# Kernel optimization log

Hardware: AMD Instinct MI355X
Metric: run time of the kernel (lower is better)

## Reference

```python
import jax, jax.numpy as jnp
import numpy as np

N_NODES = 100000
N_EDGES = 1600000
IN_CH = 64
HIDDEN = 64
OUT_DIM = HIDDEN // 2  # 32


def setup_inputs() -> dict:
    key = jax.random.key(0)
    ks = jax.random.split(key, 10)
    x = jax.random.normal(ks[0], (N_NODES, IN_CH), dtype=jnp.float32)
    edge_index = jax.random.randint(ks[1], (2, N_EDGES), 0, N_NODES, dtype=jnp.int64)
    s = 1.0 / np.sqrt(IN_CH)
    sh = 1.0 / np.sqrt(HIDDEN)
    # SAGEConv layer 1: lin_l (with bias) on aggregated neighbors, lin_r (no bias) on root
    w1l = jax.random.uniform(ks[2], (HIDDEN, IN_CH), jnp.float32, -s, s)
    b1 = jax.random.uniform(ks[3], (HIDDEN,), jnp.float32, -s, s)
    w1r = jax.random.uniform(ks[4], (HIDDEN, IN_CH), jnp.float32, -s, s)
    # SAGEConv layer 2
    w2l = jax.random.uniform(ks[5], (HIDDEN, HIDDEN), jnp.float32, -sh, sh)
    b2 = jax.random.uniform(ks[6], (HIDDEN,), jnp.float32, -sh, sh)
    w2r = jax.random.uniform(ks[7], (HIDDEN, HIDDEN), jnp.float32, -sh, sh)
    # readout head
    wh = jax.random.uniform(ks[8], (OUT_DIM, HIDDEN), jnp.float32, -sh, sh)
    bh = jax.random.uniform(ks[9], (OUT_DIM,), jnp.float32, -sh, sh)
    return {"x": x, "edge_index": edge_index, "w1l": w1l, "b1": b1, "w1r": w1r,
            "w2l": w2l, "b2": b2, "w2r": w2r, "wh": wh, "bh": bh}


def _sage_conv(h, src, dst, wl, bl, wr):
    # mean-aggregate messages from src nodes onto dst nodes
    msg = h[src]                                            # [E, d]
    agg = jax.ops.segment_sum(msg, dst, num_segments=N_NODES)  # [N, d]
    deg = jax.ops.segment_sum(jnp.ones((msg.shape[0],), h.dtype), dst,
                              num_segments=N_NODES)            # [N]
    mean = agg / jnp.maximum(deg, 1.0)[:, None]
    return mean @ wl.T + bl + h @ wr.T


def reference(x, edge_index, w1l, b1, w1r, w2l, b2, w2r, wh, bh):
    src, dst = edge_index[0], edge_index[1]
    # dropout layers are identity in eval mode
    h = jax.nn.relu(_sage_conv(x, src, dst, w1l, b1, w1r))
    h = jax.nn.relu(_sage_conv(h, src, dst, w2l, b2, w2r))
    return h @ wh.T + bh
```

## Files before the change

kernel.cpp:

```cpp
#include <hip/hip_runtime.h>


#define D 64
#define OUTD 32
#define REG_SHIFT 8
#define REG_SIZE 256
#define BCHUNK 4096
#define PADQ 16
#define CAP 5120
#define OUTCAP 8960

#define OFF_FLAG     0
#define OFF_RCUR     64
#define OFF_DEG      576
#define OFF_ROWSTART 100928
#define OFF_INV      201280
#define OFF_COL      301632
#define OFF_EBUF     3804992
#define OFF_H1B      7005056
#define OFF_MEANB    10205120
#define OFF_WC1      13405120
#define OFF_WC2      13409216
#define OFF_WHB      13413312

typedef __attribute__((ext_vector_type(8))) short bf16x8;
typedef __attribute__((ext_vector_type(4))) float f32x4;

__device__ __forceinline__ unsigned short bf16rne(float x) {
    unsigned u = __float_as_uint(x);
    unsigned r = (u + 0x7FFFu + ((u >> 16) & 1u)) >> 16;
    return (unsigned short)r;
}

__global__ void detect_init(const int* __restrict__ e32, int* __restrict__ flag,
                            int* __restrict__ rcur, int NR) {
    int t = threadIdx.x;
    if (t < 64) {
        int v = e32[2 * t + 1];
        unsigned long long m = __ballot(v != 0);
        if (t == 0) flag[0] = (m == 0ULL) ? 1 : 0;
    }
    if (t < NR) rcur[t] = t * CAP;
}

__global__ __launch_bounds__(256) void bin_edges(
        const int* __restrict__ e32, const int* __restrict__ flag,
        int* __restrict__ rcur, int* __restrict__ ebuf, int E, int NR) {
    __shared__ int stage[BCHUNK];
    __shared__ unsigned short rgn[BCHUNK];
    __shared__ int hist[512], lbase[512], startr[512], s1[512];
    int t = threadIdx.x;
    int mode = flag[0];
    int base = blockIdx.x * BCHUNK;
    for (int i = t; i < 512; i += 256) hist[i] = 0;
    __syncthreads();
    for (int j = t; j < BCHUNK; j += 256) {
        int i = base + j;
        if (i < E) {
            int d = mode ? e32[2 * (E + i)] : e32[E + i];
            atomicAdd(&hist[d >> REG_SHIFT], 1);
        }
    }
    __syncthreads();
    {
        int* a = lbase; int* b = s1;
        for (int i = t; i < 512; i += 256) a[i] = hist[i];
        __syncthreads();
        for (int off = 1; off < 512; off <<= 1) {
            for (int i = t; i < 512; i += 256)
                b[i] = a[i] + ((i >= off) ? a[i - off] : 0);
            __syncthreads();
            int* tmp = a; a = b; b = tmp;
        }
        for (int i = t; i < 512; i += 256) {
            int incl = a[i];
            int ex = incl - hist[i];
            __syncthreads();
            lbase[i] = ex;
        }
        __syncthreads();
    }
    for (int i = t; i < 512; i += 256) {
        int st = 0;
        if (i < NR && hist[i] > 0) {
            st = atomicAdd(&rcur[i], hist[i]);
            int lim = (i + 1) * CAP - hist[i];
            if (st > lim) st = lim;
        }
        startr[i] = st;
    }
    __syncthreads();
    for (int i = t; i < 512; i += 256) hist[i] = 0;
    __syncthreads();
    for (int j = t; j < BCHUNK; j += 256) {
        int i = base + j;
        if (i < E) {
            int s = mode ? e32[2 * i]       : e32[i];
            int d = mode ? e32[2 * (E + i)] : e32[E + i];
            int r = d >> REG_SHIFT;
            int o = atomicAdd(&hist[r], 1);
            int pos = lbase[r] + o;
            stage[pos] = ((d & (REG_SIZE - 1)) << 24) | s;
            rgn[pos] = (unsigned short)r;
        }
    }
    __syncthreads();
    int count = E - base; if (count > BCHUNK) count = BCHUNK;
    for (int i = t; i < count; i += 256) {
        int r = rgn[i];
        ebuf[startr[r] + (i - lbase[r])] = stage[i];
    }
}

__global__ __launch_bounds__(256) void build_csr(
        const int* __restrict__ ebuf, const int* __restrict__ rcur,
        int* __restrict__ degP, int* __restrict__ rowStartP, float* __restrict__ inv,
        int* __restrict__ colP, int N) {
    __shared__ int hist[REG_SIZE], cur[REG_SIZE], sA[REG_SIZE], sB[REG_SIZE];
    int r = blockIdx.x;
    int t = threadIdx.x;
    int lo = r << REG_SHIFT;
    int e0 = r * CAP, e1 = rcur[r];
    int colPbase = r * OUTCAP;
    hist[t] = 0;
    __syncthreads();
    for (int i = e0 + t; i < e1; i += 256)
        atomicAdd(&hist[((unsigned)ebuf[i]) >> 24], 1);
    __syncthreads();
    int v = hist[t];
    int vp = (v + PADQ - 1) & ~(PADQ - 1);
    int* a = sA; int* b = sB;
    a[t] = vp;
    __syncthreads();
    for (int off = 1; off < 256; off <<= 1) {
        b[t] = a[t] + ((t >= off) ? a[t - off] : 0);
        __syncthreads();
        int* tmp = a; a = b; b = tmp;
    }
    int startP = colPbase + (a[t] - vp);
    int node = lo + t;
    if (node < N) {
        degP[node] = vp;
        rowStartP[node] = startP;
        inv[node] = 1.0f / (float)(v > 0 ? v : 1);
    }
    cur[t] = startP;
    __syncthreads();
    for (int i = e0 + t; i < e1; i += 256) {
        int p = ebuf[i];
        int pos = atomicAdd(&cur[((unsigned)p) >> 24], 1);
        colP[pos] = (p & 0xFFFFFF) << 7;
    }
    __syncthreads();
    int zoff = N << 7;
    for (int k = startP + v; k < startP + vp; ++k) colP[k] = zoff;
}

__global__ void prep_all(const float* __restrict__ x, unsigned short* __restrict__ xb,
                         unsigned short* __restrict__ h1b,
                         const float* __restrict__ w1l, const float* __restrict__ w1r,
                         const float* __restrict__ w2l, const float* __restrict__ w2r,
                         const float* __restrict__ wh,
                         unsigned short* __restrict__ wcat1,
                         unsigned short* __restrict__ wcat2,
                         unsigned short* __restrict__ whb, int n4, int N) {
    int i = blockIdx.x * 256 + threadIdx.x;
    if (i < n4) {
        float4 v = ((const float4*)x)[i];
        unsigned lo = (unsigned)bf16rne(v.x) | ((unsigned)bf16rne(v.y) << 16);
        unsigned hi = (unsigned)bf16rne(v.z) | ((unsigned)bf16rne(v.w) << 16);
        ((uint2*)xb)[i] = make_uint2(lo, hi);
        return;
    }
    int j = i - n4;
    if (j < 16) {
        ((uint2*)xb)[(size_t)N * 16 + j] = make_uint2(0u, 0u);
    } else if (j < 32) {
        ((uint2*)h1b)[(size_t)N * 16 + (j - 16)] = make_uint2(0u, 0u);
    } else if (j < 32 + 8192) {
        int q = j - 32;
        int o = q >> 7, k = q & 127;
        wcat1[q] = bf16rne(k < 64 ? w1l[o * 64 + k] : w1r[o * 64 + k - 64]);
    } else if (j < 32 + 16384) {
        int q = j - 32 - 8192;
        int o = q >> 7, k = q & 127;
        wcat2[q] = bf16rne(k < 64 ? w2l[o * 64 + k] : w2r[o * 64 + k - 64]);
    } else if (j < 32 + 16384 + 2048) {
        int q = j - 32 - 16384;
        whb[q] = bf16rne(wh[q]);
    }
}

__global__ __launch_bounds__(256, 8) void gather_mean_bf16(
        const unsigned short* __restrict__ hb, const int* __restrict__ rowStartP,
        const int* __restrict__ degPv, const int* __restrict__ colP,
        const float* __restrict__ invdeg, unsigned short* __restrict__ meanb,
        int n) {
    int wid = (blockIdx.x * 256 + (int)threadIdx.x) >> 6;
    int lane = threadIdx.x & 63;
    if (wid >= n) return;
    int node = __builtin_amdgcn_readfirstlane(wid);

    int rs = rowStartP[node];
    int dgp = degPv[node];
    const char* hbC = (const char*)hb;

    float a0 = 0.f, a1 = 0.f, a2 = 0.f, a3 = 0.f;
    float a4 = 0.f, a5 = 0.f, a6 = 0.f, a7 = 0.f;

    for (int base = 0; base < dgp; base += 64) {
        int cv = colP[rs + base + lane];
        int m = dgp - base; if (m > 64) m = 64;
        for (int p = 0; p < m; p += 16) {
#define G(j, A) { \
            int cb = __builtin_amdgcn_readlane(cv, p + (j)); \
            const unsigned short* rp = (const unsigned short*)(hbC + cb); \
            unsigned u = rp[lane]; \
            A += __uint_as_float(u << 16); }
            G(0, a0)  G(1, a1)  G(2, a2)  G(3, a3)
            G(4, a4)  G(5, a5)  G(6, a6)  G(7, a7)
            G(8, a0)  G(9, a1)  G(10, a2) G(11, a3)
            G(12, a4) G(13, a5) G(14, a6) G(15, a7)
#undef G
        }
    }
    float s = ((a0 + a1) + (a2 + a3)) + ((a4 + a5) + (a6 + a7));
    meanb[(size_t)node * 64 + lane] = bf16rne(s * invdeg[node]);
}

template <bool HEAD>
__global__ __launch_bounds__(256, 2) void dense_mfma(
        const unsigned short* __restrict__ meanb,
        const unsigned short* __restrict__ ownb,
        const unsigned short* __restrict__ wcat,
        const float* __restrict__ bias,
        unsigned short* __restrict__ houtb,
        const unsigned short* __restrict__ whb,
        const float* __restrict__ bh,
        float* __restrict__ outp,
        int n) {
    const int lane = threadIdx.x & 63;
    const int wave = threadIdx.x >> 6;
    const int l15 = lane & 15;
    const int kg  = lane >> 4;

    bf16x8 Bf[4][4];
#pragma unroll
    for (int nt = 0; nt < 4; ++nt)
#pragma unroll
        for (int s = 0; s < 4; ++s)
            Bf[nt][s] = *(const bf16x8*)(wcat + (nt * 16 + l15) * 128 + s * 32 + kg * 8);

    float biasc[4];
#pragma unroll
    for (int nt = 0; nt < 4; ++nt) biasc[nt] = bias[nt * 16 + l15];

    bf16x8 Hf[2][2];
    float bhc[2];
    if constexpr (HEAD) {
#pragma unroll
        for (int nt = 0; nt < 2; ++nt) {
#pragma unroll
            for (int s = 0; s < 2; ++s)
                Hf[nt][s] = *(const bf16x8*)(whb + (nt * 16 + l15) * 64 + s * 32 + kg * 8);
            bhc[nt] = bh[nt * 16 + l15];
        }
    }

    __shared__ unsigned short hlds[HEAD ? 4 * 16 * 64 : 64];

    const int ntiles = (n + 15) >> 4;
    const int stride = gridDim.x * 4;
    int tile = blockIdx.x * 4 + wave;
    if (tile >= ntiles) return;

    bf16x8 Ac[4], An[4];
    {
        int row = tile * 16 + l15; if (row >= n) row = n - 1;
        const unsigned short* mrow = meanb + (size_t)row * 64 + kg * 8;
        const unsigned short* orow = ownb  + (size_t)row * 64 + kg * 8;
        Ac[0] = *(const bf16x8*)(mrow);
        Ac[1] = *(const bf16x8*)(mrow + 32);
        Ac[2] = *(const bf16x8*)(orow);
        Ac[3] = *(const bf16x8*)(orow + 32);
    }

    while (true) {
        int nxt = tile + stride;
        bool hasNext = nxt < ntiles;
        if (hasNext) {
            int row = nxt * 16 + l15; if (row >= n) row = n - 1;
            const unsigned short* mrow = meanb + (size_t)row * 64 + kg * 8;
            const unsigned short* orow = ownb  + (size_t)row * 64 + kg * 8;
            An[0] = *(const bf16x8*)(mrow);
            An[1] = *(const bf16x8*)(mrow + 32);
            An[2] = *(const bf16x8*)(orow);
            An[3] = *(const bf16x8*)(orow + 32);
        }

        f32x4 acc[4];
#pragma unroll
        for (int nt = 0; nt < 4; ++nt) {
            f32x4 a = {biasc[nt], biasc[nt], biasc[nt], biasc[nt]};
            a = __builtin_amdgcn_mfma_f32_16x16x32_bf16(Ac[0], Bf[nt][0], a, 0, 0, 0);
            a = __builtin_amdgcn_mfma_f32_16x16x32_bf16(Ac[1], Bf[nt][1], a, 0, 0, 0);
            a = __builtin_amdgcn_mfma_f32_16x16x32_bf16(Ac[2], Bf[nt][2], a, 0, 0, 0);
            a = __builtin_amdgcn_mfma_f32_16x16x32_bf16(Ac[3], Bf[nt][3], a, 0, 0, 0);
            acc[nt] = a;
        }

        int nb = tile * 16;
        if constexpr (!HEAD) {
#pragma unroll
            for (int nt = 0; nt < 4; ++nt)
#pragma unroll
                for (int r = 0; r < 4; ++r) {
                    int row = nb + kg * 4 + r;
                    float h = fmaxf(acc[nt][r], 0.0f);
                    if (row < n) houtb[(size_t)row * 64 + nt * 16 + l15] = bf16rne(h);
                }
        } else {
            unsigned short* L = hlds + wave * 1024;
            int n7 = lane & 7;
#pragma unroll
            for (int nt = 0; nt < 4; ++nt) {
                int bGlob = nt * 2 + (l15 >> 3);
#pragma unroll
                for (int r = 0; r < 4; ++r) {
                    int m = kg * 4 + r;
                    float h = fmaxf(acc[nt][r], 0.0f);
                    L[m * 64 + ((bGlob ^ (m & 7)) * 8) + n7] = bf16rne(h);
                }
            }
            __builtin_amdgcn_wave_barrier();
            bf16x8 hA[2];
#pragma unroll
            for (int s = 0; s < 2; ++s) {
                int kb = s * 4 + kg;
                hA[s] = *(const bf16x8*)(L + l15 * 64 + ((kb ^ (l15 & 7)) * 8));
            }
            __builtin_amdgcn_wave_barrier();
            f32x4 acc2[2];
#pragma unroll
            for (int nt = 0; nt < 2; ++nt) {
                f32x4 a = {bhc[nt], bhc[nt], bhc[nt], bhc[nt]};
                a = __builtin_amdgcn_mfma_f32_16x16x32_bf16(hA[0], Hf[nt][0], a, 0, 0, 0);
                a = __builtin_amdgcn_mfma_f32_16x16x32_bf16(hA[1], Hf[nt][1], a, 0, 0, 0);
                acc2[nt] = a;
            }
#pragma unroll
            for (int nt = 0; nt < 2; ++nt)
#pragma unroll
                for (int r = 0; r < 4; ++r) {
                    int row = nb + kg * 4 + r;
                    if (row < n) outp[(size_t)row * 32 + nt * 16 + l15] = acc2[nt][r];
                }
        }

        if (!hasNext) break;
        tile = nxt;
#pragma unroll
        for (int q = 0; q < 4; ++q) Ac[q] = An[q];
    }
}

extern "C" void kernel_launch(void* const* d_in, const int* in_sizes, int n_in,
                              void* d_out, int out_size, void* d_ws, size_t ws_size,
                              hipStream_t stream) {
    const float* x   = (const float*)d_in[0];
    const int* edges = (const int*)d_in[1];
    const float* w1l = (const float*)d_in[2];
    const float* b1  = (const float*)d_in[3];
    const float* w1r = (const float*)d_in[4];
    const float* w2l = (const float*)d_in[5];
    const float* b2  = (const float*)d_in[6];
    const float* w2r = (const float*)d_in[7];
    const float* wh  = (const float*)d_in[8];
    const float* bh  = (const float*)d_in[9];
    float* out = (float*)d_out;

    const int N = in_sizes[0] / D;
    const int E = in_sizes[1] / 2;
    const int NR = (N + REG_SIZE - 1) >> REG_SHIFT;

    int* ws = (int*)d_ws;
    int*            flag     = ws + OFF_FLAG;
    int*            rcur     = ws + OFF_RCUR;
    int*            degP     = ws + OFF_DEG;
    int*            rowStartP= ws + OFF_ROWSTART;
    float*          inv      = (float*)(ws + OFF_INV);
    int*            colP     = ws + OFF_COL;
    int*            ebuf     = ws + OFF_EBUF;
    unsigned short* xb       = (unsigned short*)(ws + OFF_EBUF);
    unsigned short* h1b      = (unsigned short*)(ws + OFF_H1B);
    unsigned short* meanb    = (unsigned short*)(ws + OFF_MEANB);
    unsigned short* wcat1    = (unsigned short*)(ws + OFF_WC1);
    unsigned short* wcat2    = (unsigned short*)(ws + OFF_WC2);
    unsigned short* whb      = (unsigned short*)(ws + OFF_WHB);

    detect_init<<<1, 512, 0, stream>>>(edges, flag, rcur, NR);
    int bblocks = (E + BCHUNK - 1) / BCHUNK;
    bin_edges<<<bblocks, 256, 0, stream>>>(edges, flag, rcur, ebuf, E, NR);
    build_csr<<<NR, 256, 0, stream>>>(ebuf, rcur, degP, rowStartP, inv, colP, N);

    int n4 = N * D / 4;
    prep_all<<<(n4 + 32 + 16384 + 2048 + 255) / 256, 256, 0, stream>>>(
        x, xb, h1b, w1l, w1r, w2l, w2r, wh, wcat1, wcat2, whb, n4, N);

    int gblocks = (N + 3) / 4;
    int ntiles = (N + 15) / 16;
    int dblocks = (ntiles + 7) / 8;

    gather_mean_bf16<<<gblocks, 256, 0, stream>>>(xb, rowStartP, degP, colP, inv,
                                                  meanb, N);
    dense_mfma<false><<<dblocks, 256, 0, stream>>>(meanb, xb, wcat1, b1,
                                                   h1b, nullptr, nullptr, nullptr, N);
    gather_mean_bf16<<<gblocks, 256, 0, stream>>>(h1b, rowStartP, degP, colP, inv,
                                                  meanb, N);
    dense_mfma<true><<<dblocks, 256, 0, stream>>>(meanb, h1b, wcat2, b2,
                                                  nullptr, whb, bh, out, N);
}
```

Measured before the change: 164.1 us.

## Fuse bf16 prep into edge binning kernel and gather two neighbors per wave

The separate x/weight bf16 conversion kernel is folded into the edge binning launch as extra blocks, which needs xb moved to its own workspace region so it no longer aliases ebuf. This removes one launch and lets conversion overlap with binning. The gather kernel now has each half-wave load a different neighbor row as 4-byte (two-bf16) words, so one instruction covers two edges. Each half keeps its own accumulators, and the halves are combined with a cross-half shuffle before a packed store. The costs are more accumulator registers, shuffles instead of readlanes, and a larger workspace.

```diff
diff --git a/kernel.cpp b/kernel.cpp
--- a/kernel.cpp
+++ b/kernel.cpp
@@ -17,11 +17,12 @@
 #define OFF_INV      201280
 #define OFF_COL      301632
 #define OFF_EBUF     3804992
-#define OFF_H1B      7005056
-#define OFF_MEANB    10205120
-#define OFF_WC1      13405120
-#define OFF_WC2      13409216
-#define OFF_WHB      13413312
+#define OFF_XB       5806912
+#define OFF_H1B      9006944
+#define OFF_MEANB    12206976
+#define OFF_WC1      15406976
+#define OFF_WC2      15411072
+#define OFF_WHB      15415168
 
 typedef __attribute__((ext_vector_type(8))) short bf16x8;
 typedef __attribute__((ext_vector_type(4))) float f32x4;
@@ -43,13 +44,50 @@
     if (t < NR) rcur[t] = t * CAP;
 }
 
-__global__ __launch_bounds__(256) void bin_edges(
+__global__ __launch_bounds__(256) void bin_prep(
         const int* __restrict__ e32, const int* __restrict__ flag,
-        int* __restrict__ rcur, int* __restrict__ ebuf, int E, int NR) {
+        int* __restrict__ rcur, int* __restrict__ ebuf, int E, int NR, int bblocks,
+        const float* __restrict__ x, unsigned short* __restrict__ xb,
+        unsigned short* __restrict__ h1b,
+        const float* __restrict__ w1l, const float* __restrict__ w1r,
+        const float* __restrict__ w2l, const float* __restrict__ w2r,
+        const float* __restrict__ wh,
+        unsigned short* __restrict__ wcat1, unsigned short* __restrict__ wcat2,
+        unsigned short* __restrict__ whb, int n4, int N) {
     __shared__ int stage[BCHUNK];
     __shared__ unsigned short rgn[BCHUNK];
     __shared__ int hist[512], lbase[512], startr[512], s1[512];
     int t = threadIdx.x;
+
+    if (blockIdx.x >= bblocks) {
+        int i = (blockIdx.x - bblocks) * 256 + t;
+        if (i < n4) {
+            float4 v = ((const float4*)x)[i];
+            unsigned lo = (unsigned)bf16rne(v.x) | ((unsigned)bf16rne(v.y) << 16);
+            unsigned hi = (unsigned)bf16rne(v.z) | ((unsigned)bf16rne(v.w) << 16);
+            ((uint2*)xb)[i] = make_uint2(lo, hi);
+            return;
+        }
+        int j = i - n4;
+        if (j < 16) {
+            ((uint2*)xb)[(size_t)N * 16 + j] = make_uint2(0u, 0u);
+        } else if (j < 32) {
+            ((uint2*)h1b)[(size_t)N * 16 + (j - 16)] = make_uint2(0u, 0u);
+        } else if (j < 32 + 8192) {
+            int q = j - 32;
+            int o = q >> 7, k = q & 127;
+            wcat1[q] = bf16rne(k < 64 ? w1l[o * 64 + k] : w1r[o * 64 + k - 64]);
+        } else if (j < 32 + 16384) {
+            int q = j - 32 - 8192;
+            int o = q >> 7, k = q & 127;
+            wcat2[q] = bf16rne(k < 64 ? w2l[o * 64 + k] : w2r[o * 64 + k - 64]);
+        } else if (j < 32 + 16384 + 2048) {
+            int q = j - 32 - 16384;
+            whb[q] = bf16rne(wh[q]);
+        }
+        return;
+    }
+
     int mode = flag[0];
     int base = blockIdx.x * BCHUNK;
     for (int i = t; i < 512; i += 256) hist[i] = 0;
@@ -156,41 +194,6 @@
     for (int k = startP + v; k < startP + vp; ++k) colP[k] = zoff;
 }
 
-__global__ void prep_all(const float* __restrict__ x, unsigned short* __restrict__ xb,
-                         unsigned short* __restrict__ h1b,
-                         const float* __restrict__ w1l, const float* __restrict__ w1r,
-                         const float* __restrict__ w2l, const float* __restrict__ w2r,
-                         const float* __restrict__ wh,
-                         unsigned short* __restrict__ wcat1,
-                         unsigned short* __restrict__ wcat2,
-                         unsigned short* __restrict__ whb, int n4, int N) {
-    int i = blockIdx.x * 256 + threadIdx.x;
-    if (i < n4) {
-        float4 v = ((const float4*)x)[i];
-        unsigned lo = (unsigned)bf16rne(v.x) | ((unsigned)bf16rne(v.y) << 16);
-        unsigned hi = (unsigned)bf16rne(v.z) | ((unsigned)bf16rne(v.w) << 16);
-        ((uint2*)xb)[i] = make_uint2(lo, hi);
-        return;
-    }
-    int j = i - n4;
-    if (j < 16) {
-        ((uint2*)xb)[(size_t)N * 16 + j] = make_uint2(0u, 0u);
-    } else if (j < 32) {
-        ((uint2*)h1b)[(size_t)N * 16 + (j - 16)] = make_uint2(0u, 0u);
-    } else if (j < 32 + 8192) {
-        int q = j - 32;
-        int o = q >> 7, k = q & 127;
-        wcat1[q] = bf16rne(k < 64 ? w1l[o * 64 + k] : w1r[o * 64 + k - 64]);
-    } else if (j < 32 + 16384) {
-        int q = j - 32 - 8192;
-        int o = q >> 7, k = q & 127;
-        wcat2[q] = bf16rne(k < 64 ? w2l[o * 64 + k] : w2r[o * 64 + k - 64]);
-    } else if (j < 32 + 16384 + 2048) {
-        int q = j - 32 - 16384;
-        whb[q] = bf16rne(wh[q]);
-    }
-}
-
 __global__ __launch_bounds__(256, 8) void gather_mean_bf16(
         const unsigned short* __restrict__ hb, const int* __restrict__ rowStartP,
         const int* __restrict__ degPv, const int* __restrict__ colP,
@@ -204,28 +207,38 @@
     int rs = rowStartP[node];
     int dgp = degPv[node];
     const char* hbC = (const char*)hb;
-
-    float a0 = 0.f, a1 = 0.f, a2 = 0.f, a3 = 0.f;
-    float a4 = 0.f, a5 = 0.f, a6 = 0.f, a7 = 0.f;
+    int half = lane >> 5, l31 = lane & 31;
+    int voff = l31 << 2;
+
+    float aL0 = 0.f, aL1 = 0.f, aL2 = 0.f, aL3 = 0.f;
+    float aL4 = 0.f, aL5 = 0.f, aL6 = 0.f, aL7 = 0.f;
+    float aH0 = 0.f, aH1 = 0.f, aH2 = 0.f, aH3 = 0.f;
+    float aH4 = 0.f, aH5 = 0.f, aH6 = 0.f, aH7 = 0.f;
 
     for (int base = 0; base < dgp; base += 64) {
         int cv = colP[rs + base + lane];
         int m = dgp - base; if (m > 64) m = 64;
-        for (int p = 0; p < m; p += 16) {
-#define G(j, A) { \
-            int cb = __builtin_amdgcn_readlane(cv, p + (j)); \
-            const unsigned short* rp = (const unsigned short*)(hbC + cb); \
-            unsigned u = rp[lane]; \
-            A += __uint_as_float(u << 16); }
-            G(0, a0)  G(1, a1)  G(2, a2)  G(3, a3)
-            G(4, a4)  G(5, a5)  G(6, a6)  G(7, a7)
-            G(8, a0)  G(9, a1)  G(10, a2) G(11, a3)
-            G(12, a4) G(13, a5) G(14, a6) G(15, a7)
+        int pairs = m >> 1;
+        for (int p = 0; p < pairs; p += 8) {
+#define G(j, AL, AH) { \
+            int cb = __shfl(cv, 2 * (p + (j)) + half); \
+            unsigned u = *(const unsigned*)(hbC + cb + voff); \
+            AL += __uint_as_float(u << 16); \
+            AH += __uint_as_float(u & 0xFFFF0000u); }
+            G(0, aL0, aH0)  G(1, aL1, aH1)  G(2, aL2, aH2)  G(3, aL3, aH3)
+            G(4, aL4, aH4)  G(5, aL5, aH5)  G(6, aL6, aH6)  G(7, aL7, aH7)
 #undef G
         }
     }
-    float s = ((a0 + a1) + (a2 + a3)) + ((a4 + a5) + (a6 + a7));
-    meanb[(size_t)node * 64 + lane] = bf16rne(s * invdeg[node]);
+    float s0 = ((aL0 + aL1) + (aL2 + aL3)) + ((aL4 + aL5) + (aL6 + aL7));
+    float s1 = ((aH0 + aH1) + (aH2 + aH3)) + ((aH4 + aH5) + (aH6 + aH7));
+    s0 += __shfl_xor(s0, 32);
+    s1 += __shfl_xor(s1, 32);
+    float iv = invdeg[node];
+    if (!half) {
+        unsigned mo = (unsigned)bf16rne(s0 * iv) | ((unsigned)bf16rne(s1 * iv) << 16);
+        ((unsigned*)meanb)[(size_t)node * 32 + l31] = mo;
+    }
 }
 
 template <bool HEAD>
@@ -391,7 +404,7 @@
     float*          inv      = (float*)(ws + OFF_INV);
     int*            colP     = ws + OFF_COL;
     int*            ebuf     = ws + OFF_EBUF;
-    unsigned short* xb       = (unsigned short*)(ws + OFF_EBUF);
+    unsigned short* xb       = (unsigned short*)(ws + OFF_XB);
     unsigned short* h1b      = (unsigned short*)(ws + OFF_H1B);
     unsigned short* meanb    = (unsigned short*)(ws + OFF_MEANB);
     unsigned short* wcat1    = (unsigned short*)(ws + OFF_WC1);
@@ -400,12 +413,12 @@
 
     detect_init<<<1, 512, 0, stream>>>(edges, flag, rcur, NR);
     int bblocks = (E + BCHUNK - 1) / BCHUNK;
-    bin_edges<<<bblocks, 256, 0, stream>>>(edges, flag, rcur, ebuf, E, NR);
+    int n4 = N * D / 4;
+    int pblocks = (n4 + 32 + 16384 + 2048 + 255) / 256;
+    bin_prep<<<bblocks + pblocks, 256, 0, stream>>>(
+        edges, flag, rcur, ebuf, E, NR, bblocks,
+        x, xb, h1b, w1l, w1r, w2l, w2r, wh, wcat1, wcat2, whb, n4, N);
     build_csr<<<NR, 256, 0, stream>>>(ebuf, rcur, degP, rowStartP, inv, colP, N);
-
-    int n4 = N * D / 4;
-    prep_all<<<(n4 + 32 + 16384 + 2048 + 255) / 256, 256, 0, stream>>>(
-        x, xb, h1b, w1l, w1r, w2l, w2r, wh, wcat1, wcat2, whb, n4, N);
 
     int gblocks = (N + 3) / 4;
     int ntiles = (N + 15) / 16;
```

After: 155.9 us. -5.0%, faster.
